# Kernel optimization log

Measured on AMD Instinct MI355X. Metric: run time of the kernel, lower is better.

The kernel has to match this reference:

```python
import jax, jax.numpy as jnp
import numpy as np

BS, D = 4096, 768

def setup_inputs() -> dict:
    key = jax.random.key(0)
    k1, k2 = jax.random.split(key)
    code_vec = jax.random.normal(k1, (BS, D), dtype=jnp.float32)
    nl_vec = jax.random.normal(k2, (BS, D), dtype=jnp.float32)
    return {"code_vec": code_vec, "nl_vec": nl_vec, "bs": BS}

def reference(code_vec, nl_vec, bs):
    # scores[i, j] = <nl_vec[i], code_vec[j]>  -- expressed as a GEMM
    scores = jnp.einsum("nd,md->nm", nl_vec, code_vec)  # [bs, bs]
    # CrossEntropyLoss with labels = arange(bs): mean of -log_softmax diagonal
    logprobs = jax.nn.log_softmax(scores, axis=-1)
    labels = jnp.arange(bs)
    loss = -jnp.mean(logprobs[labels, labels])
    return loss
```

## Files before the change

### kernel.cpp

```cpp
#include <hip/hip_runtime.h>
#include <hip/hip_bf16.h>
#include <math.h>

#define BSZ 4096
#define DIM 768
#define BK 64
#define NTILE (DIM / BK)
#define CSPLIT 16
#define NPANEL 32

typedef __attribute__((ext_vector_type(8))) short short8;
typedef __attribute__((ext_vector_type(4))) float f32x4;

__device__ __forceinline__ unsigned short f2bf(float f) {
  unsigned u = __float_as_uint(f);
  u += 0x7fffu + ((u >> 16) & 1u);
  return (unsigned short)(u >> 16);
}

__device__ __forceinline__ void gload16(const void* gp, const void* lp) {
  __builtin_amdgcn_global_load_lds(
      (const __attribute__((address_space(1))) unsigned int*)(size_t)gp,
      (__attribute__((address_space(3))) unsigned int*)(unsigned int)(size_t)lp,
      16, 0, 0);
}

__device__ __forceinline__ short8 lds_ld(const unsigned char* p) {
  return *(const short8*)p;
}

__device__ __forceinline__ void cstore(float* p, float v) {
  __hip_atomic_store(p, v, __ATOMIC_RELAXED, __HIP_MEMORY_SCOPE_AGENT);
}
__device__ __forceinline__ float cload(const float* p) {
  return __hip_atomic_load(p, __ATOMIC_RELAXED, __HIP_MEMORY_SCOPE_AGENT);
}

__global__ void convert_kernel(const float* __restrict__ src0,
                               const float* __restrict__ src1,
                               unsigned short* __restrict__ dst0,
                               unsigned short* __restrict__ dst1,
                               unsigned int* __restrict__ cnt)
{
  if (blockIdx.x == 0 && threadIdx.x <= NPANEL) cnt[threadIdx.x] = 0u;
  const int n4 = (BSZ * DIM) / 4;
  int i = blockIdx.x * blockDim.x + threadIdx.x;
  const float* src;
  unsigned short* dst;
  if (i < n4) { src = src0; dst = dst0; }
  else        { src = src1; dst = dst1; i -= n4; }
  float4 v = *reinterpret_cast<const float4*>(src + (size_t)i * 4);
  ushort4 o;
  o.x = f2bf(v.x); o.y = f2bf(v.y); o.z = f2bf(v.z); o.w = f2bf(v.w);
  *reinterpret_cast<ushort4*>(dst + (size_t)i * 4) = o;
}

__global__ __launch_bounds__(512, 2)
void gemm_lse_kernel(const unsigned short* __restrict__ A,
                     const unsigned short* __restrict__ B,
                     float* __restrict__ pm, float* __restrict__ ps,
                     float* __restrict__ diag,
                     float* __restrict__ partial,
                     unsigned int* __restrict__ cnt,
                     float* __restrict__ out)
{
  __shared__ alignas(16) unsigned char smem[98304];
  const int tid  = threadIdx.x;
  const int w    = tid >> 6;
  const int lane = tid & 63;
  const int lr   = lane & 15;
  const int hi   = lane >> 4;
  const int wm   = w >> 2;
  const int wn   = w & 3;

  const int g   = blockIdx.y * 32 + blockIdx.x;
  const int xcd = g & 7;
  const int t   = g >> 3;
  const int rnd = t >> 5;
  const int s   = t & 31;
  const int bxl = s & 7, byl = s >> 3;
  const int bx  = ((xcd & 3) << 3) | bxl;
  const int by  = ((xcd >> 2) << 3) | (rnd << 2) | byl;
  const int i0  = bx << 7;
  const int j0  = by << 8;

  const int fb0 = (hi ^ (lr & 7)) << 4;
  const int fb1 = ((4 + hi) ^ (lr & 7)) << 4;
  const int arowb = (wm * 64 + lr) * 128;
  const int browb = (wn * 64 + lr) * 128;

  const int srow = tid >> 3;
  const int gcol = ((tid & 7) ^ (srow & 7)) << 3;
  const unsigned short* pA = A + (size_t)(i0 + srow) * DIM + gcol;
  const unsigned short* pB = B + (size_t)(j0 + srow) * DIM + gcol;
  const int ldsbase = w << 10;

  f32x4 acc[4][4];
#pragma unroll
  for (int m = 0; m < 4; ++m)
#pragma unroll
    for (int n = 0; n < 4; ++n)
      acc[m][n] = (f32x4){0.f, 0.f, 0.f, 0.f};

  gload16(pA,                      smem +        ldsbase);
  gload16(pA + (size_t)64 * DIM,   smem + 8192 + ldsbase);
#pragma unroll
  for (int q = 0; q < 4; ++q)
    gload16(pB + (size_t)(q * 64) * DIM, smem + 32768 + q * 8192 + ldsbase);
  asm volatile("s_waitcnt vmcnt(0)" ::: "memory");
  __builtin_amdgcn_s_barrier();

#pragma unroll 2
  for (int u = 0; u < NTILE; ++u) {
    const int c = u & 1;
    const unsigned char* la = smem + c * 16384;
    const unsigned char* lb = smem + 32768 + c * 32768;
    unsigned char* na = smem + (c ^ 1) * 16384;
    unsigned char* nb = smem + 32768 + (c ^ 1) * 32768;
    const bool st = (u + 1 < NTILE);
    const size_t kn = (size_t)(u + 1) * BK;

    short8 aF[4], bF[4];

#pragma unroll
    for (int n = 0; n < 4; ++n) bF[n] = lds_ld(lb + browb + n * 2048 + fb0);
#pragma unroll
    for (int m = 0; m < 4; ++m) aF[m] = lds_ld(la + arowb + m * 2048 + fb0);
    if (st) {
      gload16(pB + kn,                     nb + ldsbase);
      gload16(pB + (size_t) 64 * DIM + kn, nb +     8192 + ldsbase);
      gload16(pB + (size_t)128 * DIM + kn, nb + 2 * 8192 + ldsbase);
      gload16(pB + (size_t)192 * DIM + kn, nb + 3 * 8192 + ldsbase);
      gload16(pA + kn,                     na + ldsbase);
      gload16(pA + (size_t) 64 * DIM + kn, na +     8192 + ldsbase);
    }
    __builtin_amdgcn_s_barrier();
    asm volatile("s_waitcnt lgkmcnt(0)" ::: "memory");
    __builtin_amdgcn_s_setprio(1);
#pragma unroll
    for (int m = 0; m < 4; ++m)
#pragma unroll
      for (int n = 0; n < 4; ++n)
        acc[m][n] = __builtin_amdgcn_mfma_f32_16x16x32_bf16(aF[m], bF[n], acc[m][n], 0, 0, 0);
    __builtin_amdgcn_s_setprio(0);
    __builtin_amdgcn_s_barrier();

#pragma unroll
    for (int n = 0; n < 4; ++n) bF[n] = lds_ld(lb + browb + n * 2048 + fb1);
#pragma unroll
    for (int m = 0; m < 4; ++m) aF[m] = lds_ld(la + arowb + m * 2048 + fb1);
    __builtin_amdgcn_s_barrier();
    asm volatile("s_waitcnt lgkmcnt(0)" ::: "memory");
    __builtin_amdgcn_s_setprio(1);
#pragma unroll
    for (int m = 0; m < 4; ++m)
#pragma unroll
      for (int n = 0; n < 4; ++n)
        acc[m][n] = __builtin_amdgcn_mfma_f32_16x16x32_bf16(aF[m], bF[n], acc[m][n], 0, 0, 0);
    __builtin_amdgcn_s_setprio(0);
    asm volatile("s_waitcnt vmcnt(0)" ::: "memory");
    __builtin_amdgcn_s_barrier();
  }

  __syncthreads();

  const int dof = i0 - j0;
  if (dof >= 0 && dof < 256) {
#pragma unroll
    for (int m = 0; m < 4; ++m)
#pragma unroll
      for (int n = 0; n < 4; ++n)
#pragma unroll
        for (int rr = 0; rr < 4; ++rr) {
          const int rl = wm * 64 + m * 16 + (hi << 2) + rr;
          const int cl = wn * 64 + n * 16 + lr;
          if (cl == rl + dof) cstore(&diag[i0 + rl], acc[m][n][rr]);
        }
  }

  float* redm = (float*)smem;
  float* reds = (float*)(smem + 2048);

#pragma unroll
  for (int m = 0; m < 4; ++m) {
    float mx[4], sm[4];
#pragma unroll
    for (int rr = 0; rr < 4; ++rr) {
      float v = fmaxf(fmaxf(acc[m][0][rr], acc[m][1][rr]),
                      fmaxf(acc[m][2][rr], acc[m][3][rr]));
      mx[rr] = v;
    }
#pragma unroll
    for (int sh = 1; sh < 16; sh <<= 1)
#pragma unroll
      for (int rr = 0; rr < 4; ++rr)
        mx[rr] = fmaxf(mx[rr], __shfl_xor(mx[rr], sh, 64));
#pragma unroll
    for (int rr = 0; rr < 4; ++rr) {
      float s = 0.f;
#pragma unroll
      for (int n = 0; n < 4; ++n) s += __expf(acc[m][n][rr] - mx[rr]);
      sm[rr] = s;
    }
#pragma unroll
    for (int sh = 1; sh < 16; sh <<= 1)
#pragma unroll
      for (int rr = 0; rr < 4; ++rr)
        sm[rr] += __shfl_xor(sm[rr], sh, 64);
    if (lr == 0) {
#pragma unroll
      for (int rr = 0; rr < 4; ++rr) {
        const int rl = wm * 64 + m * 16 + (hi << 2) + rr;
        redm[(wn << 7) + rl] = mx[rr];
        reds[(wn << 7) + rl] = sm[rr];
      }
    }
  }
  __syncthreads();

  if (tid < 128) {
    float m = redm[tid];
#pragma unroll
    for (int v = 1; v < 4; ++v) m = fmaxf(m, redm[(v << 7) + tid]);
    float s = 0.f;
#pragma unroll
    for (int v = 0; v < 4; ++v) s += reds[(v << 7) + tid] * __expf(redm[(v << 7) + tid] - m);
    cstore(&pm[(size_t)by * BSZ + i0 + tid], m);
    cstore(&ps[(size_t)by * BSZ + i0 + tid], s);
  }

  asm volatile("s_waitcnt vmcnt(0)" ::: "memory");
  __syncthreads();
  __shared__ unsigned int sord;
  if (tid == 0) sord = atomicAdd(&cnt[bx], 1u);
  __syncthreads();
  if (sord == CSPLIT - 1) {
    float val = 0.f;
    if (tid < 128) {
      const int row = i0 + tid;
      float mv[CSPLIT];
      float m = -INFINITY;
#pragma unroll
      for (int c = 0; c < CSPLIT; ++c) {
        mv[c] = cload(&pm[(size_t)c * BSZ + row]);
        m = fmaxf(m, mv[c]);
      }
      float s = 0.f;
#pragma unroll
      for (int c = 0; c < CSPLIT; ++c)
        s += cload(&ps[(size_t)c * BSZ + row]) * __expf(mv[c] - m);
      val = (m + __logf(s)) - cload(&diag[row]);
    }
    float* red2 = (float*)smem;
    red2[tid] = val;
    __syncthreads();
    for (int off = 256; off > 0; off >>= 1) {
      if (tid < off) red2[tid] += red2[tid + off];
      __syncthreads();
    }
    if (tid == 0) {
      cstore(&partial[bx], red2[0]);
      asm volatile("s_waitcnt vmcnt(0)" ::: "memory");
      unsigned int d = atomicAdd(&cnt[NPANEL], 1u);
      if (d == NPANEL - 1) {
        float s = 0.f;
        for (int i = 0; i < NPANEL; ++i) s += cload(&partial[i]);
        out[0] = s / (float)BSZ;
      }
    }
  }
}

extern "C" void kernel_launch(void* const* d_in, const int* in_sizes, int n_in,
                              void* d_out, int out_size, void* d_ws, size_t ws_size,
                              hipStream_t stream) {
  const float* code = (const float*)d_in[0];
  const float* nl   = (const float*)d_in[1];
  float* out = (float*)d_out;

  char* ws = (char*)d_ws;
  unsigned short* Abf = (unsigned short*)ws;
  unsigned short* Bbf = (unsigned short*)(ws + (size_t)BSZ * DIM * 2);
  float* pm   = (float*)(ws + (size_t)BSZ * DIM * 4);
  float* ps   = pm + (size_t)CSPLIT * BSZ;
  float* diag = ps + (size_t)CSPLIT * BSZ;
  float* partial = diag + BSZ;
  unsigned int* cnt = (unsigned int*)(partial + NPANEL);

  const int n4 = (BSZ * DIM) / 4;
  convert_kernel<<<(2 * n4) / 256, 256, 0, stream>>>(nl, code, Abf, Bbf, cnt);

  dim3 grid(BSZ / 128, BSZ / 256);
  gemm_lse_kernel<<<grid, 512, 0, stream>>>(Abf, Bbf, pm, ps, diag, partial, cnt, out);
}
```

Baseline: 52.26 us.

## Switch GEMM mainloop to triple-buffered BK=32 pipeline with higher occupancy

Halves the K tile to 32, uses three LDS buffers with a prefetch distance of two tiles, and waits with partial vmcnt instead of draining all loads each iteration. The smaller LDS footprint (72KB) and launch bounds of 4 waves-per-EU aim at more resident work and fewer barriers per K-step, and the block-to-tile remap for XCD locality is simplified. Risks include register pressure from the tighter launch bound, a changed swizzle that may add LDS bank conflicts, and more loop iterations with less MFMA work per barrier.

After: 53.38 us. +2.2%, slower.

```diff
diff --git a/kernel.cpp b/kernel.cpp
--- a/kernel.cpp
+++ b/kernel.cpp
@@ -4,10 +4,11 @@
 
 #define BSZ 4096
 #define DIM 768
-#define BK 64
+#define BK 32
 #define NTILE (DIM / BK)
 #define CSPLIT 16
 #define NPANEL 32
+#define BUFSZ 24576
 
 typedef __attribute__((ext_vector_type(8))) short short8;
 typedef __attribute__((ext_vector_type(4))) float f32x4;
@@ -55,7 +56,7 @@
   *reinterpret_cast<ushort4*>(dst + (size_t)i * 4) = o;
 }
 
-__global__ __launch_bounds__(512, 2)
+__global__ __launch_bounds__(512, 4)
 void gemm_lse_kernel(const unsigned short* __restrict__ A,
                      const unsigned short* __restrict__ B,
                      float* __restrict__ pm, float* __restrict__ ps,
@@ -64,7 +65,7 @@
                      unsigned int* __restrict__ cnt,
                      float* __restrict__ out)
 {
-  __shared__ alignas(16) unsigned char smem[98304];
+  __shared__ alignas(16) unsigned char smem[3 * BUFSZ];
   const int tid  = threadIdx.x;
   const int w    = tid >> 6;
   const int lane = tid & 63;
@@ -76,21 +77,17 @@
   const int g   = blockIdx.y * 32 + blockIdx.x;
   const int xcd = g & 7;
   const int t   = g >> 3;
-  const int rnd = t >> 5;
-  const int s   = t & 31;
-  const int bxl = s & 7, byl = s >> 3;
-  const int bx  = ((xcd & 3) << 3) | bxl;
-  const int by  = ((xcd >> 2) << 3) | (rnd << 2) | byl;
+  const int bx  = ((xcd & 3) << 3) | (t & 7);
+  const int by  = ((xcd >> 2) << 3) | (t >> 3);
   const int i0  = bx << 7;
   const int j0  = by << 8;
 
-  const int fb0 = (hi ^ (lr & 7)) << 4;
-  const int fb1 = ((4 + hi) ^ (lr & 7)) << 4;
-  const int arowb = (wm * 64 + lr) * 128;
-  const int browb = (wn * 64 + lr) * 128;
-
-  const int srow = tid >> 3;
-  const int gcol = ((tid & 7) ^ (srow & 7)) << 3;
+  const int fb    = (hi ^ ((lr >> 1) & 3)) << 4;
+  const int arowb = (wm * 64 + lr) * 64;
+  const int browb = (wn * 64 + lr) * 64;
+
+  const int srow = tid >> 2;
+  const int gcol = (((tid & 3) ^ ((tid >> 3) & 3)) << 3);
   const unsigned short* pA = A + (size_t)(i0 + srow) * DIM + gcol;
   const unsigned short* pB = B + (size_t)(j0 + srow) * DIM + gcol;
   const int ldsbase = w << 10;
@@ -102,39 +99,32 @@
     for (int n = 0; n < 4; ++n)
       acc[m][n] = (f32x4){0.f, 0.f, 0.f, 0.f};
 
-  gload16(pA,                      smem +        ldsbase);
-  gload16(pA + (size_t)64 * DIM,   smem + 8192 + ldsbase);
-#pragma unroll
-  for (int q = 0; q < 4; ++q)
-    gload16(pB + (size_t)(q * 64) * DIM, smem + 32768 + q * 8192 + ldsbase);
-  asm volatile("s_waitcnt vmcnt(0)" ::: "memory");
+  gload16(pB,                          smem +  8192 + ldsbase);
+  gload16(pB + (size_t)128 * DIM,      smem + 16384 + ldsbase);
+  gload16(pA,                          smem +         ldsbase);
+  gload16(pB + BK,                     smem + BUFSZ +  8192 + ldsbase);
+  gload16(pB + (size_t)128 * DIM + BK, smem + BUFSZ + 16384 + ldsbase);
+  gload16(pA + BK,                     smem + BUFSZ +         ldsbase);
+  asm volatile("s_waitcnt vmcnt(3)" ::: "memory");
   __builtin_amdgcn_s_barrier();
 
-#pragma unroll 2
+#pragma unroll 3
   for (int u = 0; u < NTILE; ++u) {
-    const int c = u & 1;
-    const unsigned char* la = smem + c * 16384;
-    const unsigned char* lb = smem + 32768 + c * 32768;
-    unsigned char* na = smem + (c ^ 1) * 16384;
-    unsigned char* nb = smem + 32768 + (c ^ 1) * 32768;
-    const bool st = (u + 1 < NTILE);
-    const size_t kn = (size_t)(u + 1) * BK;
+    const unsigned char* lv = smem + (u % 3) * BUFSZ;
+    unsigned char* nv = smem + ((u + 2) % 3) * BUFSZ;
+    const bool st = (u + 2 < NTILE);
+    const size_t kn = (size_t)(u + 2) * BK;
 
     short8 aF[4], bF[4];
-
-#pragma unroll
-    for (int n = 0; n < 4; ++n) bF[n] = lds_ld(lb + browb + n * 2048 + fb0);
-#pragma unroll
-    for (int m = 0; m < 4; ++m) aF[m] = lds_ld(la + arowb + m * 2048 + fb0);
+#pragma unroll
+    for (int n = 0; n < 4; ++n) bF[n] = lds_ld(lv + 8192 + browb + n * 1024 + fb);
+#pragma unroll
+    for (int m = 0; m < 4; ++m) aF[m] = lds_ld(lv + arowb + m * 1024 + fb);
     if (st) {
-      gload16(pB + kn,                     nb + ldsbase);
-      gload16(pB + (size_t) 64 * DIM + kn, nb +     8192 + ldsbase);
-      gload16(pB + (size_t)128 * DIM + kn, nb + 2 * 8192 + ldsbase);
-      gload16(pB + (size_t)192 * DIM + kn, nb + 3 * 8192 + ldsbase);
-      gload16(pA + kn,                     na + ldsbase);
-      gload16(pA + (size_t) 64 * DIM + kn, na +     8192 + ldsbase);
-    }
-    __builtin_amdgcn_s_barrier();
+      gload16(pB + kn,                     nv +  8192 + ldsbase);
+      gload16(pB + (size_t)128 * DIM + kn, nv + 16384 + ldsbase);
+      gload16(pA + kn,                     nv +         ldsbase);
+    }
     asm volatile("s_waitcnt lgkmcnt(0)" ::: "memory");
     __builtin_amdgcn_s_setprio(1);
 #pragma unroll
@@ -143,22 +133,8 @@
       for (int n = 0; n < 4; ++n)
         acc[m][n] = __builtin_amdgcn_mfma_f32_16x16x32_bf16(aF[m], bF[n], acc[m][n], 0, 0, 0);
     __builtin_amdgcn_s_setprio(0);
-    __builtin_amdgcn_s_barrier();
-
-#pragma unroll
-    for (int n = 0; n < 4; ++n) bF[n] = lds_ld(lb + browb + n * 2048 + fb1);
-#pragma unroll
-    for (int m = 0; m < 4; ++m) aF[m] = lds_ld(la + arowb + m * 2048 + fb1);
-    __builtin_amdgcn_s_barrier();
-    asm volatile("s_waitcnt lgkmcnt(0)" ::: "memory");
-    __builtin_amdgcn_s_setprio(1);
-#pragma unroll
-    for (int m = 0; m < 4; ++m)
-#pragma unroll
-      for (int n = 0; n < 4; ++n)
-        acc[m][n] = __builtin_amdgcn_mfma_f32_16x16x32_bf16(aF[m], bF[n], acc[m][n], 0, 0, 0);
-    __builtin_amdgcn_s_setprio(0);
-    asm volatile("s_waitcnt vmcnt(0)" ::: "memory");
+    if (st) asm volatile("s_waitcnt vmcnt(3)" ::: "memory");
+    else    asm volatile("s_waitcnt vmcnt(0)" ::: "memory");
     __builtin_amdgcn_s_barrier();
   }
 
```
